# Performance work log

Hardware: AMD Instinct MI355X
Metric: run time of the kernel (lower is better)

Reference implementation:

```python
import jax, jax.numpy as jnp
import numpy as np

N = 50000
E = 500000
HID = 64
HEADS = 4
LAYERS = 4
CDIM = 8


def _p(key, shape, scale=0.05):
    return jax.random.normal(key, shape, dtype=jnp.float32) * scale


def setup_inputs() -> dict:
    key = jax.random.key(0)
    ks = jax.random.split(key, 32)
    x = jax.random.normal(ks[0], (N, 8), dtype=jnp.float32)
    src = jax.random.randint(ks[1], (E,), 0, N)
    dst = jax.random.randint(ks[2], (E,), 0, N)
    edge_index = jnp.stack([src, dst]).astype(jnp.int64)
    HC = HEADS * HID
    inp = {
        "x": x,
        "edge_index": edge_index,
        # encoder: Linear(8,64), ELU, Linear(64,64), ELU
        "enc_w1": _p(ks[3], (HID, 8)), "enc_b1": _p(ks[4], (HID,)),
        "enc_w2": _p(ks[5], (HID, HID)), "enc_b2": _p(ks[6], (HID,)),
        # per-layer TransformerConv params, stacked over layers
        "Wq": _p(ks[7], (LAYERS, HC, HID)), "bq": _p(ks[8], (LAYERS, HC)),
        "Wk": _p(ks[9], (LAYERS, HC, HID)), "bk": _p(ks[10], (LAYERS, HC)),
        "Wv": _p(ks[11], (LAYERS, HC, HID)), "bv": _p(ks[12], (LAYERS, HC)),
        "Ws": _p(ks[13], (LAYERS, HID, HID)), "bs": _p(ks[14], (LAYERS, HID)),
        # output MLP: 64->64->32->8
        "out_w1": _p(ks[15], (64, HID)), "out_b1": _p(ks[16], (64,)),
        "out_w2": _p(ks[17], (32, 64)), "out_b2": _p(ks[18], (32,)),
        "out_w3": _p(ks[19], (CDIM, 32)), "out_b3": _p(ks[20], (CDIM,)),
    }
    return inp


def transformer_conv(h, src, dst, Wq, bq, Wk, bk, Wv, bv, Ws, bs):
    """PyG TransformerConv, concat=False, root_weight=True, eval mode (no dropout)."""
    n = h.shape[0]
    q = (h @ Wq.T + bq).reshape(n, HEADS, HID)
    k = (h @ Wk.T + bk).reshape(n, HEADS, HID)
    v = (h @ Wv.T + bv).reshape(n, HEADS, HID)
    # per-edge multi-head scores: (E, H)
    alpha = jnp.einsum("ehd,ehd->eh", q[dst], k[src]) / np.sqrt(HID).astype(np.float32)
    # segment softmax over edges grouped by destination node
    amax = jax.ops.segment_max(alpha, dst, num_segments=n)          # (N, H)
    ex = jnp.exp(alpha - amax[dst])                                 # (E, H)
    denom = jax.ops.segment_sum(ex, dst, num_segments=n)           # (N, H)
    w = ex / denom[dst]                                             # (E, H)
    msg = v[src] * w[:, :, None]                                    # (E, H, C)
    agg = jax.ops.segment_sum(msg, dst, num_segments=n)            # (N, H, C)
    out = agg.mean(axis=1)                                          # concat=False -> head mean
    return out + h @ Ws.T + bs                                      # skip connection


def reference(x, edge_index, enc_w1, enc_b1, enc_w2, enc_b2,
              Wq, bq, Wk, bk, Wv, bv, Ws, bs,
              out_w1, out_b1, out_w2, out_b2, out_w3, out_b3):
    src, dst = edge_index[0], edge_index[1]
    elu = jax.nn.elu
    h = elu(x @ enc_w1.T + enc_b1)
    h = elu(h @ enc_w2.T + enc_b2)
    for l in range(LAYERS):
        h = elu(transformer_conv(h, src, dst, Wq[l], bq[l], Wk[l], bk[l],
                                 Wv[l], bv[l], Ws[l], bs[l]))
        # dropout is identity in eval mode
    o = elu(h @ out_w1.T + out_b1)
    o = elu(o @ out_w2.T + out_b2)
    o = o @ out_w3.T + out_b3
    return o
```

## Files before the change

### kernel.cpp

```cpp
#include <hip/hip_runtime.h>
#include <hip/hip_bf16.h>

#define N_NODES 50000
#define N_EDGES 500000
constexpr int HID = 64;
constexpr int HC  = 256;

typedef unsigned short u16;
typedef unsigned char u8;
typedef __attribute__((ext_vector_type(8))) __bf16 bf16x8;
typedef __attribute__((ext_vector_type(4))) float f32x4;
typedef __attribute__((ext_vector_type(2))) float f32x2;

__device__ __forceinline__ float b2f(u16 u) {
    union { unsigned int i; float f; } c; c.i = ((unsigned int)u) << 16; return c.f;
}
__device__ __forceinline__ u16 f2b(float f) {
    union { float f; unsigned int i; } c; c.f = f;
    unsigned int x = c.i;
    unsigned int lsb = (x >> 16) & 1u;
    x += 0x7fffu + lsb;
    return (u16)(x >> 16);
}
__device__ __forceinline__ float elu_f(float x) { return x > 0.f ? x : expm1f(x); }


__global__ __launch_bounds__(256) void init_kernel(int* __restrict__ cnt, int* __restrict__ cursor,
                                                   int* __restrict__ csr) {
    int i = blockIdx.x * 256 + threadIdx.x;
    if (i < N_NODES) { cnt[i] = 0; cursor[i] = 0; }
    if (blockIdx.x == 0 && threadIdx.x < 8) csr[N_EDGES + threadIdx.x] = 0;
}

__global__ __launch_bounds__(256) void detect_kernel(const int* __restrict__ ei, int* __restrict__ flag) {
    __shared__ int s[4];
    int t = threadIdx.x;
    int nz = ei[2 * t + 1] != 0;
    unsigned long long m = __ballot(nz);
    if ((t & 63) == 0) s[t >> 6] = (m != 0ull) ? 1 : 0;
    __syncthreads();
    if (t == 0) flag[0] = s[0] | s[1] | s[2] | s[3];
}

__global__ __launch_bounds__(256) void wcvt_kernel(const float* __restrict__ Wq, const float* __restrict__ Wk,
                                                   const float* __restrict__ Wv, const float* __restrict__ Wsk,
                                                   u16* __restrict__ w16) {
    int i = blockIdx.x * 256 + threadIdx.x;
    if (i >= 53248) return;
    const float* src; int off;
    if (i < 16384)      { src = Wq;  off = i; }
    else if (i < 32768) { src = Wk;  off = i - 16384; }
    else if (i < 49152) { src = Wv;  off = i - 32768; }
    else                { src = Wsk; off = i - 49152; }
    float4 v = ((const float4*)src)[off];
    ushort4 u; u.x = f2b(v.x); u.y = f2b(v.y); u.z = f2b(v.z); u.w = f2b(v.w);
    ((ushort4*)w16)[i] = u;
}

__global__ __launch_bounds__(256) void hist_kernel(const int* __restrict__ ei, const int* __restrict__ flag,
                                                   int* __restrict__ cnt) {
    int e = blockIdx.x * 256 + threadIdx.x;
    if (e < N_EDGES) {
        int d = flag[0] ? ei[N_EDGES + e] : ei[2 * N_EDGES + 2 * e];
        atomicAdd(&cnt[d], 1);
    }
}

__global__ __launch_bounds__(512) void scan1_kernel(const int* __restrict__ cnt,
                                                    int* __restrict__ row_start, int* __restrict__ bsum) {
    __shared__ int sc[512];
    int t = threadIdx.x;
    int i = blockIdx.x * 512 + t;
    int v = (i < N_NODES) ? cnt[i] : 0;
    sc[t] = v;
    __syncthreads();
    for (int off = 1; off < 512; off <<= 1) {
        int u = (t >= off) ? sc[t - off] : 0;
        __syncthreads();
        sc[t] += u;
        __syncthreads();
    }
    if (i < N_NODES) row_start[i] = sc[t] - v;
    if (t == 511) bsum[blockIdx.x] = sc[511];
}

__global__ __launch_bounds__(128) void scan2_kernel(int* __restrict__ bsum, int* __restrict__ row_start) {
    __shared__ int sc[128];
    const int NB = (N_NODES + 511) / 512;
    int t = threadIdx.x;
    int v = (t < NB) ? bsum[t] : 0;
    sc[t] = v;
    __syncthreads();
    for (int off = 1; off < 128; off <<= 1) {
        int u = (t >= off) ? sc[t - off] : 0;
        __syncthreads();
        sc[t] += u;
        __syncthreads();
    }
    if (t < NB) bsum[t] = sc[t] - v;
    if (t == 127) row_start[N_NODES] = sc[127];
}

__global__ __launch_bounds__(512) void scan3_kernel(int* __restrict__ row_start, const int* __restrict__ bsum) {
    int i = blockIdx.x * 512 + threadIdx.x;
    if (i < N_NODES) row_start[i] += bsum[blockIdx.x];
}

__global__ __launch_bounds__(256) void scatter_kernel(const int* __restrict__ ei, const int* __restrict__ flag,
                                const int* __restrict__ row_start, int* __restrict__ cursor,
                                int* __restrict__ csr_src) {
    int e = blockIdx.x * 256 + threadIdx.x;
    if (e < N_EDGES) {
        int isI32 = flag[0];
        int s = isI32 ? ei[e] : ei[2 * e];
        int d = isI32 ? ei[N_EDGES + e] : ei[2 * N_EDGES + 2 * e];
        int pos = row_start[d] + atomicAdd(&cursor[d], 1);
        csr_src[pos] = s;
    }
}

__global__ __launch_bounds__(256) void encoder_kernel(const float* __restrict__ x,
                               const float* __restrict__ w1, const float* __restrict__ b1,
                               const float* __restrict__ w2, const float* __restrict__ b2,
                               float* __restrict__ h) {
    __shared__ float xs[64 * 9];
    __shared__ float w1s[64 * 9];
    __shared__ u16 t1s[64 * 72];
    __shared__ u16 w2s[64 * 72];
    __shared__ float b1s[64], b2s[64];
    int t = threadIdx.x;
    int m0 = blockIdx.x * 64;

    if (t < 128) {
        int row = t >> 1, c = (t & 1) * 4;
        float4 val = make_float4(0.f, 0.f, 0.f, 0.f);
        if (m0 + row < N_NODES) val = *(const float4*)(x + (size_t)(m0 + row) * 8 + c);
        *(float4*)&xs[row * 9 + c] = val;
    }
    if (t >= 128 && t < 256) {
        int p = t - 128;
        int row = p >> 1, c = (p & 1) * 4;
        float4 val = *(const float4*)(w1 + row * 8 + c);
        *(float4*)&w1s[row * 9 + c] = val;
    }
    #pragma unroll
    for (int r = 0; r < 4; ++r) {
        int p = t + r * 256; int row = p >> 4, kc = (p & 15) * 4;
        float4 val = *(const float4*)(w2 + row * 64 + kc);
        ushort4 u; u.x = f2b(val.x); u.y = f2b(val.y); u.z = f2b(val.z); u.w = f2b(val.w);
        *(ushort4*)&w2s[row * 72 + kc] = u;
    }
    if (t < 64) { b1s[t] = b1[t]; b2s[t] = b2[t]; }
    __syncthreads();

    {
        int j = t & 63, sub = t >> 6;
        #pragma unroll
        for (int g = 0; g < 16; ++g) {
            int node = g * 4 + sub;
            float acc = b1s[j];
            #pragma unroll
            for (int m = 0; m < 8; ++m) acc += xs[node * 9 + m] * w1s[j * 9 + m];
            t1s[node * 72 + j] = f2b(elu_f(acc));
        }
    }
    __syncthreads();

    int wave = t >> 6, lane = t & 63;
    int lrow = lane & 15, quad = lane >> 4;
    int m_off = wave * 16;
    bf16x8 a0 = *(const bf16x8*)&t1s[(m_off + lrow) * 72 + quad * 8];
    bf16x8 a1 = *(const bf16x8*)&t1s[(m_off + lrow) * 72 + 32 + quad * 8];
    #pragma unroll
    for (int nsub = 0; nsub < 4; ++nsub) {
        bf16x8 b0 = *(const bf16x8*)&w2s[(nsub * 16 + lrow) * 72 + quad * 8];
        bf16x8 b1v = *(const bf16x8*)&w2s[(nsub * 16 + lrow) * 72 + 32 + quad * 8];
        f32x4 acc = {0.f, 0.f, 0.f, 0.f};
        acc = __builtin_amdgcn_mfma_f32_16x16x32_bf16(a0, b0, acc, 0, 0, 0);
        acc = __builtin_amdgcn_mfma_f32_16x16x32_bf16(a1, b1v, acc, 0, 0, 0);
        int col = nsub * 16 + lrow;
        float bias = b2s[col];
        #pragma unroll
        for (int r = 0; r < 4; ++r) {
            int row = m0 + m_off + quad * 4 + r;
            if (row < N_NODES) h[(size_t)row * 64 + col] = elu_f(acc[r] + bias);
        }
    }
}

__global__ __launch_bounds__(256) void proj_kernel(const float* __restrict__ h,
    const u16* __restrict__ wq16, const u16* __restrict__ wk16,
    const u16* __restrict__ wv16, const u16* __restrict__ wsk16,
    const float* __restrict__ bq, const float* __restrict__ bk,
    const float* __restrict__ bv, const float* __restrict__ bsk,
    int layer,
    u16* __restrict__ q, u8* __restrict__ kv, float* __restrict__ skip)
{
    __shared__ u16 as_tile[64 * 72];
    __shared__ u16 ws_tile[64 * 72];
    __shared__ float pool[64 * 68];
    u16* qst  = (u16*)pool;
    u8*  kvst = (u8*)pool;
    float* skst = pool;

    int t = threadIdx.x;
    int m0 = blockIdx.x * 64;

    #pragma unroll
    for (int r = 0; r < 4; ++r) {
        int p = t + r * 256; int row = p >> 4, kc = (p & 15) * 4;
        float4 val = make_float4(0.f, 0.f, 0.f, 0.f);
        if (m0 + row < N_NODES) val = *(const float4*)(h + (size_t)(m0 + row) * 64 + kc);
        ushort4 u; u.x = f2b(val.x); u.y = f2b(val.y); u.z = f2b(val.z); u.w = f2b(val.w);
        *(ushort4*)&as_tile[row * 72 + kc] = u;
    }
    __syncthreads();

    int wave = t >> 6, lane = t & 63;
    int lrow = lane & 15, quad = lane >> 4;
    bf16x8 a0 = *(const bf16x8*)&as_tile[(wave * 16 + lrow) * 72 + quad * 8];
    bf16x8 a1 = *(const bf16x8*)&as_tile[(wave * 16 + lrow) * 72 + 32 + quad * 8];

    const u16* Wq16  = wq16  + (size_t)layer * HC * HID;
    const u16* Wk16  = wk16  + (size_t)layer * HC * HID;
    const u16* Wv16  = wv16  + (size_t)layer * HC * HID;
    const u16* Wsk16 = wsk16 + (size_t)layer * HID * HID;
    const float* bqL  = bq  + layer * HC;
    const float* bkL  = bk  + layer * HC;
    const float* bvL  = bv  + layer * HC;
    const float* bskL = bsk + layer * HID;

    int nl = wave * 16 + lrow;

    auto tile_base = [&](int idx) -> const u16* {
        if (idx < 4) return Wq16 + (size_t)(idx * 64) * 64;
        if (idx < 12) {
            int p2 = idx - 4; int ctk = p2 >> 1;
            return ((p2 & 1) ? Wv16 : Wk16) + (size_t)(ctk * 64) * 64;
        }
        return Wsk16;
    };

    int p0 = t, p1 = t + 256;
    int g_off0 = (p0 >> 3) * 64 + (p0 & 7) * 8;
    int g_off1 = (p1 >> 3) * 64 + (p1 & 7) * 8;
    int l_off0 = (p0 >> 3) * 72 + (p0 & 7) * 8;
    int l_off1 = (p1 >> 3) * 72 + (p1 & 7) * 8;

    uint4 pre0 = *(const uint4*)(tile_base(0) + g_off0);
    uint4 pre1 = *(const uint4*)(tile_base(0) + g_off1);

    for (int idx = 0; idx < 13; ++idx) {
        const float* bt; int cbase; int mode;
        if (idx < 4)       { bt = bqL + idx * 64; cbase = idx * 64; mode = 0; }
        else if (idx < 12) { int p2 = idx - 4; int ctk = p2 >> 1; cbase = ctk * 64;
                             if ((p2 & 1) == 0) { bt = bkL + cbase; mode = 1; }
                             else               { bt = bvL + cbase; mode = 2; } }
        else               { bt = bskL; cbase = 0; mode = 3; }

        __syncthreads();
        *(uint4*)&ws_tile[l_off0] = pre0;
        *(uint4*)&ws_tile[l_off1] = pre1;
        if (idx + 1 < 13) {
            pre0 = *(const uint4*)(tile_base(idx + 1) + g_off0);
            pre1 = *(const uint4*)(tile_base(idx + 1) + g_off1);
        }
        __syncthreads();

        #pragma unroll
        for (int nsub = 0; nsub < 4; ++nsub) {
            bf16x8 w0 = *(const bf16x8*)&ws_tile[(nsub * 16 + lrow) * 72 + quad * 8];
            bf16x8 w1 = *(const bf16x8*)&ws_tile[(nsub * 16 + lrow) * 72 + 32 + quad * 8];
            f32x4 acc = {0.f, 0.f, 0.f, 0.f};
            acc = __builtin_amdgcn_mfma_f32_16x16x32_bf16(w0, a0, acc, 0, 0, 0);
            acc = __builtin_amdgcn_mfma_f32_16x16x32_bf16(w1, a1, acc, 0, 0, 0);
            float4 b4 = *(const float4*)(bt + nsub * 16 + quad * 4);
            if (mode == 0) {
                ushort4 o;
                o.x = f2b(acc[0] + b4.x); o.y = f2b(acc[1] + b4.y);
                o.z = f2b(acc[2] + b4.z); o.w = f2b(acc[3] + b4.w);
                *(ushort4*)&qst[nl * 72 + nsub * 16 + quad * 4] = o;
            } else if (mode == 1 || mode == 2) {
                float f0 = (acc[0] + b4.x) * 16.f, f1 = (acc[1] + b4.y) * 16.f;
                float f2v = (acc[2] + b4.z) * 16.f, f3v = (acc[3] + b4.w) * 16.f;
                int pk = __builtin_amdgcn_cvt_pk_fp8_f32(f0, f1, 0, false);
                pk = __builtin_amdgcn_cvt_pk_fp8_f32(f2v, f3v, pk, true);
                int g = nsub * 4 + quad;
                *(unsigned int*)&kvst[nl * 144 + g * 8 + (mode == 2 ? 4 : 0)] = (unsigned int)pk;
            } else {
                float4 o;
                o.x = acc[0] + b4.x; o.y = acc[1] + b4.y;
                o.z = acc[2] + b4.z; o.w = acc[3] + b4.w;
                *(float4*)&skst[nl * 68 + nsub * 16 + quad * 4] = o;
            }
        }

        if (mode == 0) {
            __syncthreads();
            #pragma unroll
            for (int it = 0; it < 2; ++it) {
                int p = t + it * 256; int row = p >> 3, ch = p & 7;
                int grow = m0 + row;
                if (grow < N_NODES)
                    *(uint4*)(q + (size_t)grow * 256 + cbase + ch * 8) = *(const uint4*)&qst[row * 72 + ch * 8];
            }
        } else if (mode == 2) {
            __syncthreads();
            #pragma unroll
            for (int it = 0; it < 2; ++it) {
                int p = t + it * 256; int row = p >> 3, ch = p & 7;
                int grow = m0 + row;
                if (grow < N_NODES)
                    *(uint4*)(kv + (size_t)grow * 512 + cbase * 2 + ch * 16) = *(const uint4*)&kvst[row * 144 + ch * 16];
            }
        } else if (mode == 3) {
            __syncthreads();
            int row = t >> 2, c0 = (t & 3) * 16;
            int grow = m0 + row;
            if (grow < N_NODES) {
                #pragma unroll
                for (int j = 0; j < 4; ++j)
                    *(float4*)(skip + (size_t)grow * 64 + c0 + j * 4) = *(const float4*)&skst[row * 68 + c0 + j * 4];
            }
        }
    }
}

__global__ __launch_bounds__(256) void attn_kernel(
    const u16* __restrict__ q, const u8* __restrict__ kv,
    const float* __restrict__ skip,
    const int* __restrict__ row_start, const int* __restrict__ csr_src,
    float* __restrict__ hout)
{
    int wave = threadIdx.x >> 6;
    int lane = threadIdx.x & 63;
    int n = blockIdx.x * 4 + wave;
    if (n >= N_NODES) return;
    const float SC = 0.0078125f * 1.44269504f;
    ushort4 q4 = ((const ushort4*)(q + (size_t)n * 256))[lane];
    float qf0 = b2f(q4.x) * SC, qf1 = b2f(q4.y) * SC, qf2 = b2f(q4.z) * SC, qf3 = b2f(q4.w) * SC;
    const u8* kvl = kv + lane * 8;
    float l = 0.f;
    float a0 = 0.f, a1 = 0.f, a2 = 0.f, a3 = 0.f;
    int e0 = row_start[n], e1 = row_start[n + 1];
    for (int e = e0; e < e1; e += 4) {
        int rem = e1 - e;
        int s0 = csr_src[e], s1 = csr_src[e + 1], s2 = csr_src[e + 2], s3 = csr_src[e + 3];
        uint2 c0 = *(const uint2*)(kvl + (size_t)s0 * 512);
        uint2 c1 = *(const uint2*)(kvl + (size_t)s1 * 512);
        uint2 c2 = *(const uint2*)(kvl + (size_t)s2 * 512);
        uint2 c3 = *(const uint2*)(kvl + (size_t)s3 * 512);
        f32x2 k0a = __builtin_amdgcn_cvt_pk_f32_fp8(c0.x, false), k0b = __builtin_amdgcn_cvt_pk_f32_fp8(c0.x, true);
        f32x2 k1a = __builtin_amdgcn_cvt_pk_f32_fp8(c1.x, false), k1b = __builtin_amdgcn_cvt_pk_f32_fp8(c1.x, true);
        f32x2 k2a = __builtin_amdgcn_cvt_pk_f32_fp8(c2.x, false), k2b = __builtin_amdgcn_cvt_pk_f32_fp8(c2.x, true);
        f32x2 k3a = __builtin_amdgcn_cvt_pk_f32_fp8(c3.x, false), k3b = __builtin_amdgcn_cvt_pk_f32_fp8(c3.x, true);
        float p0 = qf0 * k0a.x + qf1 * k0a.y + qf2 * k0b.x + qf3 * k0b.y;
        float p1 = qf0 * k1a.x + qf1 * k1a.y + qf2 * k1b.x + qf3 * k1b.y;
        float p2 = qf0 * k2a.x + qf1 * k2a.y + qf2 * k2b.x + qf3 * k2b.y;
        float p3 = qf0 * k3a.x + qf1 * k3a.y + qf2 * k3b.x + qf3 * k3b.y;
        p0 += __shfl_xor(p0, 1); p1 += __shfl_xor(p1, 1); p2 += __shfl_xor(p2, 1); p3 += __shfl_xor(p3, 1);
        p0 += __shfl_xor(p0, 2); p1 += __shfl_xor(p1, 2); p2 += __shfl_xor(p2, 2); p3 += __shfl_xor(p3, 2);
        p0 += __shfl_xor(p0, 4); p1 += __shfl_xor(p1, 4); p2 += __shfl_xor(p2, 4); p3 += __shfl_xor(p3, 4);
        p0 += __shfl_xor(p0, 8); p1 += __shfl_xor(p1, 8); p2 += __shfl_xor(p2, 8); p3 += __shfl_xor(p3, 8);
        float w0 = exp2f(p0);
        float w1 = rem > 1 ? exp2f(p1) : 0.f;
        float w2 = rem > 2 ? exp2f(p2) : 0.f;
        float w3 = rem > 3 ? exp2f(p3) : 0.f;
        l += (w0 + w1) + (w2 + w3);
        f32x2 v0a = __builtin_amdgcn_cvt_pk_f32_fp8(c0.y, false), v0b = __builtin_amdgcn_cvt_pk_f32_fp8(c0.y, true);
        f32x2 v1a = __builtin_amdgcn_cvt_pk_f32_fp8(c1.y, false), v1b = __builtin_amdgcn_cvt_pk_f32_fp8(c1.y, true);
        f32x2 v2a = __builtin_amdgcn_cvt_pk_f32_fp8(c2.y, false), v2b = __builtin_amdgcn_cvt_pk_f32_fp8(c2.y, true);
        f32x2 v3a = __builtin_amdgcn_cvt_pk_f32_fp8(c3.y, false), v3b = __builtin_amdgcn_cvt_pk_f32_fp8(c3.y, true);
        a0 += w0 * v0a.x + w1 * v1a.x + w2 * v2a.x + w3 * v3a.x;
        a1 += w0 * v0a.y + w1 * v1a.y + w2 * v2a.y + w3 * v3a.y;
        a2 += w0 * v0b.x + w1 * v1b.x + w2 * v2b.x + w3 * v3b.x;
        a3 += w0 * v0b.y + w1 * v1b.y + w2 * v2b.y + w3 * v3b.y;
    }
    float inv = l > 0.f ? 1.f / l : 0.f;
    a0 *= inv; a1 *= inv; a2 *= inv; a3 *= inv;
    a0 += __shfl_xor(a0, 16); a0 += __shfl_xor(a0, 32);
    a1 += __shfl_xor(a1, 16); a1 += __shfl_xor(a1, 32);
    a2 += __shfl_xor(a2, 16); a2 += __shfl_xor(a2, 32);
    a3 += __shfl_xor(a3, 16); a3 += __shfl_xor(a3, 32);
    if ((lane >> 4) == 0) {
        const float OS = 0.015625f;
        float4 sk = ((const float4*)(skip + (size_t)n * 64))[lane];
        float4 o;
        o.x = elu_f(OS * a0 + sk.x);
        o.y = elu_f(OS * a1 + sk.y);
        o.z = elu_f(OS * a2 + sk.z);
        o.w = elu_f(OS * a3 + sk.w);
        ((float4*)(hout + (size_t)n * 64))[lane] = o;
    }
}

__global__ __launch_bounds__(256) void mlp_kernel(const float* __restrict__ h,
    const float* __restrict__ w1, const float* __restrict__ b1,
    const float* __restrict__ w2, const float* __restrict__ b2,
    const float* __restrict__ w3, const float* __restrict__ b3,
    float* __restrict__ out)
{
    __shared__ u16 hs[64 * 72];
    __shared__ u16 w1s[64 * 72];
    __shared__ u16 t1s[64 * 72];
    __shared__ u16 w2s[32 * 72];
    __shared__ float t2s[64 * 33];
    __shared__ float w3s[8 * 33];
    __shared__ float b1s[64], b2s[32], b3s[8];
    int t = threadIdx.x;
    int m0 = blockIdx.x * 64;

    #pragma unroll
    for (int r = 0; r < 4; ++r) {
        int p = t + r * 256; int row = p >> 4, kc = (p & 15) * 4;
        float4 val = make_float4(0.f, 0.f, 0.f, 0.f);
        if (m0 + row < N_NODES) val = *(const float4*)(h + (size_t)(m0 + row) * 64 + kc);
        ushort4 u; u.x = f2b(val.x); u.y = f2b(val.y); u.z = f2b(val.z); u.w = f2b(val.w);
        *(ushort4*)&hs[row * 72 + kc] = u;
    }
    #pragma unroll
    for (int r = 0; r < 4; ++r) {
        int p = t + r * 256; int row = p >> 4, kc = (p & 15) * 4;
        float4 val = *(const float4*)(w1 + row * 64 + kc);
        ushort4 u; u.x = f2b(val.x); u.y = f2b(val.y); u.z = f2b(val.z); u.w = f2b(val.w);
        *(ushort4*)&w1s[row * 72 + kc] = u;
    }
    #pragma unroll
    for (int r = 0; r < 2; ++r) {
        int p = t + r * 256; int row = p >> 4, kc = (p & 15) * 4;
        float4 val = *(const float4*)(w2 + row * 64 + kc);
        ushort4 u; u.x = f2b(val.x); u.y = f2b(val.y); u.z = f2b(val.z); u.w = f2b(val.w);
        *(ushort4*)&w2s[row * 72 + kc] = u;
    }
    if (t < 8 * 32) { int r = t >> 5, c = t & 31; w3s[r * 33 + c] = w3[t]; }
    if (t < 64) b1s[t] = b1[t];
    if (t >= 64 && t < 96) b2s[t - 64] = b2[t - 64];
    if (t >= 96 && t < 104) b3s[t - 96] = b3[t - 96];
    __syncthreads();

    int wave = t >> 6, lane = t & 63;
    int lrow = lane & 15, quad = lane >> 4;
    int m_off = wave * 16;

    {
        bf16x8 a0 = *(const bf16x8*)&hs[(m_off + lrow) * 72 + quad * 8];
        bf16x8 a1 = *(const bf16x8*)&hs[(m_off + lrow) * 72 + 32 + quad * 8];
        #pragma unroll
        for (int nsub = 0; nsub < 4; ++nsub) {
            bf16x8 b0 = *(const bf16x8*)&w1s[(nsub * 16 + lrow) * 72 + quad * 8];
            bf16x8 b1v = *(const bf16x8*)&w1s[(nsub * 16 + lrow) * 72 + 32 + quad * 8];
            f32x4 acc = {0.f, 0.f, 0.f, 0.f};
            acc = __builtin_amdgcn_mfma_f32_16x16x32_bf16(a0, b0, acc, 0, 0, 0);
            acc = __builtin_amdgcn_mfma_f32_16x16x32_bf16(a1, b1v, acc, 0, 0, 0);
            int col = nsub * 16 + lrow;
            float bias = b1s[col];
            #pragma unroll
            for (int r = 0; r < 4; ++r) {
                int row = m_off + quad * 4 + r;
                t1s[row * 72 + col] = f2b(elu_f(acc[r] + bias));
            }
        }
    }
    __syncthreads();

    {
        bf16x8 a0 = *(const bf16x8*)&t1s[(m_off + lrow) * 72 + quad * 8];
        bf16x8 a1 = *(const bf16x8*)&t1s[(m_off + lrow) * 72 + 32 + quad * 8];
        #pragma unroll
        for (int nsub = 0; nsub < 2; ++nsub) {
            bf16x8 b0 = *(const bf16x8*)&w2s[(nsub * 16 + lrow) * 72 + quad * 8];
            bf16x8 b1v = *(const bf16x8*)&w2s[(nsub * 16 + lrow) * 72 + 32 + quad * 8];
            f32x4 acc = {0.f, 0.f, 0.f, 0.f};
            acc = __builtin_amdgcn_mfma_f32_16x16x32_bf16(a0, b0, acc, 0, 0, 0);
            acc = __builtin_amdgcn_mfma_f32_16x16x32_bf16(a1, b1v, acc, 0, 0, 0);
            int col = nsub * 16 + lrow;
            float bias = b2s[col];
            #pragma unroll
            for (int r = 0; r < 4; ++r) {
                int row = m_off + quad * 4 + r;
                t2s[row * 33 + col] = elu_f(acc[r] + bias);
            }
        }
    }
    __syncthreads();

    #pragma unroll
    for (int r = 0; r < 2; ++r) {
        int idx = t + r * 256;
        int node = idx >> 3, j = idx & 7;
        int row = m0 + node;
        if (row < N_NODES) {
            float acc = b3s[j];
            #pragma unroll
            for (int kk = 0; kk < 32; ++kk) acc += t2s[node * 33 + kk] * w3s[j * 33 + kk];
            out[(size_t)row * 8 + j] = acc;
        }
    }
}

extern "C" void kernel_launch(void* const* d_in, const int* in_sizes, int n_in,
                              void* d_out, int out_size, void* d_ws, size_t ws_size,
                              hipStream_t stream) {
    (void)in_sizes; (void)n_in; (void)out_size; (void)ws_size;
    const float* x   = (const float*)d_in[0];
    const int* ei    = (const int*)d_in[1];
    const float* ew1 = (const float*)d_in[2];
    const float* eb1 = (const float*)d_in[3];
    const float* ew2 = (const float*)d_in[4];
    const float* eb2 = (const float*)d_in[5];
    const float* Wq  = (const float*)d_in[6];
    const float* bq  = (const float*)d_in[7];
    const float* Wk  = (const float*)d_in[8];
    const float* bk  = (const float*)d_in[9];
    const float* Wv  = (const float*)d_in[10];
    const float* bv  = (const float*)d_in[11];
    const float* Wsk = (const float*)d_in[12];
    const float* bsk = (const float*)d_in[13];
    const float* ow1 = (const float*)d_in[14];
    const float* ob1 = (const float*)d_in[15];
    const float* ow2 = (const float*)d_in[16];
    const float* ob2 = (const float*)d_in[17];
    const float* ow3 = (const float*)d_in[18];
    const float* ob3 = (const float*)d_in[19];

    char* ws = (char*)d_ws;
    size_t off = 0;
    auto alloc = [&](size_t bytes) -> void* {
        void* p = ws + off;
        off += (bytes + 255) & ~(size_t)255;
        return p;
    };
    float* h0    = (float*)alloc((size_t)N_NODES * 64 * 4);
    float* h1    = (float*)alloc((size_t)N_NODES * 64 * 4);
    u16*   q     = (u16*)  alloc((size_t)N_NODES * 256 * 2);
    u8*    kv    = (u8*)   alloc((size_t)N_NODES * 512);
    float* skp   = (float*)alloc((size_t)N_NODES * 64 * 4);
    u16*   w16   = (u16*)  alloc((size_t)212992 * 2);
    int*   cnt   = (int*)  alloc((size_t)N_NODES * 4);
    int*   cursor= (int*)  alloc((size_t)N_NODES * 4);
    int*   rowst = (int*)  alloc((size_t)(N_NODES + 1) * 4);
    int*   csr   = (int*)  alloc((size_t)(N_EDGES + 8) * 4);
    int*   bsum  = (int*)  alloc(512);
    int*   flag  = (int*)  alloc(256);

    u16* wq16  = w16;
    u16* wk16  = w16 + 65536;
    u16* wv16  = w16 + 131072;
    u16* wsk16 = w16 + 196608;

    const int NB = (N_NODES + 511) / 512;

    init_kernel<<<(N_NODES + 255) / 256, 256, 0, stream>>>(cnt, cursor, csr);
    detect_kernel<<<1, 256, 0, stream>>>(ei, flag);
    wcvt_kernel<<<208, 256, 0, stream>>>(Wq, Wk, Wv, Wsk, w16);
    hist_kernel<<<(N_EDGES + 255) / 256, 256, 0, stream>>>(ei, flag, cnt);
    scan1_kernel<<<NB, 512, 0, stream>>>(cnt, rowst, bsum);
    scan2_kernel<<<1, 128, 0, stream>>>(bsum, rowst);
    scan3_kernel<<<NB, 512, 0, stream>>>(rowst, bsum);
    scatter_kernel<<<(N_EDGES + 255) / 256, 256, 0, stream>>>(ei, flag, rowst, cursor, csr);

    encoder_kernel<<<(N_NODES + 63) / 64, 256, 0, stream>>>(x, ew1, eb1, ew2, eb2, h0);

    float* hin = h0;
    float* hout = h1;
    for (int l = 0; l < 4; ++l) {
        proj_kernel<<<(N_NODES + 63) / 64, 256, 0, stream>>>(hin, wq16, wk16, wv16, wsk16,
                                                             bq, bk, bv, bsk, l, q, kv, skp);
        attn_kernel<<<(N_NODES + 3) / 4, 256, 0, stream>>>(q, kv, skp, rowst, csr, hout);
        float* tmp = hin; hin = hout; hout = tmp;
    }

    mlp_kernel<<<(N_NODES + 63) / 64, 256, 0, stream>>>(hin, ow1, ob1, ow2, ob2, ow3, ob3, (float*)d_out);
}
```

Measured before the change: 491.8 us.

## Process two degree-sorted nodes per wave in attention kernel

Adds a counting sort of nodes by in-degree (histogram, scan, scatter into a permutation) and changes the attention kernel so each 64-lane wave handles two nodes, one per 32-lane half. Each lane now loads 16 bytes of K/V and 8 query values per edge. Pairing nodes of similar degree is meant to limit divergence between the two halves while halving the number of waves and the per-edge shuffle depth. The cost is three extra small preprocessing kernels, an indirect node lookup, and scattered output writes in permuted order.

```diff
diff --git a/kernel.cpp b/kernel.cpp
--- a/kernel.cpp
+++ b/kernel.cpp
@@ -26,10 +26,12 @@
 
 
 __global__ __launch_bounds__(256) void init_kernel(int* __restrict__ cnt, int* __restrict__ cursor,
-                                                   int* __restrict__ csr) {
+                                                   int* __restrict__ csr,
+                                                   int* __restrict__ dbins, int* __restrict__ dcur) {
     int i = blockIdx.x * 256 + threadIdx.x;
     if (i < N_NODES) { cnt[i] = 0; cursor[i] = 0; }
     if (blockIdx.x == 0 && threadIdx.x < 8) csr[N_EDGES + threadIdx.x] = 0;
+    if (blockIdx.x == 0 && threadIdx.x < 64) { dbins[threadIdx.x] = 0; dcur[threadIdx.x] = 0; }
 }
 
 __global__ __launch_bounds__(256) void detect_kernel(const int* __restrict__ ei, int* __restrict__ flag) {
@@ -116,6 +118,41 @@
         int d = isI32 ? ei[N_EDGES + e] : ei[2 * N_EDGES + 2 * e];
         int pos = row_start[d] + atomicAdd(&cursor[d], 1);
         csr_src[pos] = s;
+    }
+}
+
+__global__ __launch_bounds__(256) void dhist_kernel(const int* __restrict__ cnt, int* __restrict__ dbins) {
+    __shared__ int lb[64];
+    int t = threadIdx.x;
+    if (t < 64) lb[t] = 0;
+    __syncthreads();
+    int i = blockIdx.x * 256 + t;
+    if (i < N_NODES) {
+        int d = cnt[i]; if (d > 63) d = 63;
+        atomicAdd(&lb[d], 1);
+    }
+    __syncthreads();
+    if (t < 64 && lb[t]) atomicAdd(&dbins[t], lb[t]);
+}
+
+__global__ __launch_bounds__(64) void dscan_kernel(const int* __restrict__ dbins, int* __restrict__ doffs) {
+    int t = threadIdx.x;
+    int v = dbins[t];
+    int s = v;
+    for (int off = 1; off < 64; off <<= 1) {
+        int u = __shfl_up(s, off);
+        if (t >= off) s += u;
+    }
+    doffs[t] = s - v;
+}
+
+__global__ __launch_bounds__(256) void dscatter_kernel(const int* __restrict__ cnt, const int* __restrict__ doffs,
+                                                       int* __restrict__ dcur, int* __restrict__ perm) {
+    int i = blockIdx.x * 256 + threadIdx.x;
+    if (i < N_NODES) {
+        int d = cnt[i]; if (d > 63) d = 63;
+        int pos = doffs[d] + atomicAdd(&dcur[d], 1);
+        perm[pos] = i;
     }
 }
 
@@ -330,67 +367,116 @@
     const u16* __restrict__ q, const u8* __restrict__ kv,
     const float* __restrict__ skip,
     const int* __restrict__ row_start, const int* __restrict__ csr_src,
+    const int* __restrict__ perm,
     float* __restrict__ hout)
 {
     int wave = threadIdx.x >> 6;
     int lane = threadIdx.x & 63;
-    int n = blockIdx.x * 4 + wave;
-    if (n >= N_NODES) return;
+    int half = lane >> 5;
+    int l32 = lane & 31;
+    int gw = blockIdx.x * 4 + wave;
+    int slot = 2 * gw + half;
+    bool valid = slot < N_NODES;
+    int n = valid ? perm[slot] : 0;
+
     const float SC = 0.0078125f * 1.44269504f;
-    ushort4 q4 = ((const ushort4*)(q + (size_t)n * 256))[lane];
-    float qf0 = b2f(q4.x) * SC, qf1 = b2f(q4.y) * SC, qf2 = b2f(q4.z) * SC, qf3 = b2f(q4.w) * SC;
-    const u8* kvl = kv + lane * 8;
+    float qf[8];
+    {
+        uint4 qr = *(const uint4*)(q + (size_t)n * 256 + l32 * 8);
+        const u16* qp = (const u16*)&qr;
+        #pragma unroll
+        for (int j = 0; j < 8; ++j) qf[j] = b2f(qp[j]) * SC;
+    }
+    int e0 = valid ? row_start[n] : 0;
+    int e1 = valid ? row_start[n + 1] : 0;
+    int ng = (e1 - e0 + 3) >> 2;
+    int ngo = __shfl_xor(ng, 32);
+    int ngmax = ng > ngo ? ng : ngo;
+    int elast = (e1 - 1 > e0) ? e1 - 1 : e0;
+
+    const u8* kvl = kv + l32 * 16;
     float l = 0.f;
-    float a0 = 0.f, a1 = 0.f, a2 = 0.f, a3 = 0.f;
-    int e0 = row_start[n], e1 = row_start[n + 1];
-    for (int e = e0; e < e1; e += 4) {
+    float a[8] = {};
+    for (int i = 0; i < ngmax; ++i) {
+        int e = e0 + 4 * i;
         int rem = e1 - e;
-        int s0 = csr_src[e], s1 = csr_src[e + 1], s2 = csr_src[e + 2], s3 = csr_src[e + 3];
-        uint2 c0 = *(const uint2*)(kvl + (size_t)s0 * 512);
-        uint2 c1 = *(const uint2*)(kvl + (size_t)s1 * 512);
-        uint2 c2 = *(const uint2*)(kvl + (size_t)s2 * 512);
-        uint2 c3 = *(const uint2*)(kvl + (size_t)s3 * 512);
-        f32x2 k0a = __builtin_amdgcn_cvt_pk_f32_fp8(c0.x, false), k0b = __builtin_amdgcn_cvt_pk_f32_fp8(c0.x, true);
-        f32x2 k1a = __builtin_amdgcn_cvt_pk_f32_fp8(c1.x, false), k1b = __builtin_amdgcn_cvt_pk_f32_fp8(c1.x, true);
-        f32x2 k2a = __builtin_amdgcn_cvt_pk_f32_fp8(c2.x, false), k2b = __builtin_amdgcn_cvt_pk_f32_fp8(c2.x, true);
-        f32x2 k3a = __builtin_amdgcn_cvt_pk_f32_fp8(c3.x, false), k3b = __builtin_amdgcn_cvt_pk_f32_fp8(c3.x, true);
-        float p0 = qf0 * k0a.x + qf1 * k0a.y + qf2 * k0b.x + qf3 * k0b.y;
-        float p1 = qf0 * k1a.x + qf1 * k1a.y + qf2 * k1b.x + qf3 * k1b.y;
-        float p2 = qf0 * k2a.x + qf1 * k2a.y + qf2 * k2b.x + qf3 * k2b.y;
-        float p3 = qf0 * k3a.x + qf1 * k3a.y + qf2 * k3b.x + qf3 * k3b.y;
+        int i0 = e     <= elast ? e     : elast;
+        int i1 = e + 1 <= elast ? e + 1 : elast;
+        int i2 = e + 2 <= elast ? e + 2 : elast;
+        int i3 = e + 3 <= elast ? e + 3 : elast;
+        int s0 = csr_src[i0], s1 = csr_src[i1], s2 = csr_src[i2], s3 = csr_src[i3];
+        uint4 c0 = *(const uint4*)(kvl + (size_t)s0 * 512);
+        uint4 c1 = *(const uint4*)(kvl + (size_t)s1 * 512);
+        uint4 c2 = *(const uint4*)(kvl + (size_t)s2 * 512);
+        uint4 c3 = *(const uint4*)(kvl + (size_t)s3 * 512);
+        float p0, p1, p2, p3;
+        {
+            f32x2 ka, kb, kc, kd;
+            ka = __builtin_amdgcn_cvt_pk_f32_fp8(c0.x, false); kb = __builtin_amdgcn_cvt_pk_f32_fp8(c0.x, true);
+            kc = __builtin_amdgcn_cvt_pk_f32_fp8(c0.z, false); kd = __builtin_amdgcn_cvt_pk_f32_fp8(c0.z, true);
+            p0 = qf[0]*ka.x + qf[1]*ka.y + qf[2]*kb.x + qf[3]*kb.y + qf[4]*kc.x + qf[5]*kc.y + qf[6]*kd.x + qf[7]*kd.y;
+            ka = __builtin_amdgcn_cvt_pk_f32_fp8(c1.x, false); kb = __builtin_amdgcn_cvt_pk_f32_fp8(c1.x, true);
+            kc = __builtin_amdgcn_cvt_pk_f32_fp8(c1.z, false); kd = __builtin_amdgcn_cvt_pk_f32_fp8(c1.z, true);
+            p1 = qf[0]*ka.x + qf[1]*ka.y + qf[2]*kb.x + qf[3]*kb.y + qf[4]*kc.x + qf[5]*kc.y + qf[6]*kd.x + qf[7]*kd.y;
+            ka = __builtin_amdgcn_cvt_pk_f32_fp8(c2.x, false); kb = __builtin_amdgcn_cvt_pk_f32_fp8(c2.x, true);
+            kc = __builtin_amdgcn_cvt_pk_f32_fp8(c2.z, false); kd = __builtin_amdgcn_cvt_pk_f32_fp8(c2.z, true);
+            p2 = qf[0]*ka.x + qf[1]*ka.y + qf[2]*kb.x + qf[3]*kb.y + qf[4]*kc.x + qf[5]*kc.y + qf[6]*kd.x + qf[7]*kd.y;
+            ka = __builtin_amdgcn_cvt_pk_f32_fp8(c3.x, false); kb = __builtin_amdgcn_cvt_pk_f32_fp8(c3.x, true);
+            kc = __builtin_amdgcn_cvt_pk_f32_fp8(c3.z, false); kd = __builtin_amdgcn_cvt_pk_f32_fp8(c3.z, true);
+            p3 = qf[0]*ka.x + qf[1]*ka.y + qf[2]*kb.x + qf[3]*kb.y + qf[4]*kc.x + qf[5]*kc.y + qf[6]*kd.x + qf[7]*kd.y;
+        }
         p0 += __shfl_xor(p0, 1); p1 += __shfl_xor(p1, 1); p2 += __shfl_xor(p2, 1); p3 += __shfl_xor(p3, 1);
         p0 += __shfl_xor(p0, 2); p1 += __shfl_xor(p1, 2); p2 += __shfl_xor(p2, 2); p3 += __shfl_xor(p3, 2);
         p0 += __shfl_xor(p0, 4); p1 += __shfl_xor(p1, 4); p2 += __shfl_xor(p2, 4); p3 += __shfl_xor(p3, 4);
-        p0 += __shfl_xor(p0, 8); p1 += __shfl_xor(p1, 8); p2 += __shfl_xor(p2, 8); p3 += __shfl_xor(p3, 8);
-        float w0 = exp2f(p0);
+        float w0 = rem > 0 ? exp2f(p0) : 0.f;
         float w1 = rem > 1 ? exp2f(p1) : 0.f;
         float w2 = rem > 2 ? exp2f(p2) : 0.f;
         float w3 = rem > 3 ? exp2f(p3) : 0.f;
         l += (w0 + w1) + (w2 + w3);
-        f32x2 v0a = __builtin_amdgcn_cvt_pk_f32_fp8(c0.y, false), v0b = __builtin_amdgcn_cvt_pk_f32_fp8(c0.y, true);
-        f32x2 v1a = __builtin_amdgcn_cvt_pk_f32_fp8(c1.y, false), v1b = __builtin_amdgcn_cvt_pk_f32_fp8(c1.y, true);
-        f32x2 v2a = __builtin_amdgcn_cvt_pk_f32_fp8(c2.y, false), v2b = __builtin_amdgcn_cvt_pk_f32_fp8(c2.y, true);
-        f32x2 v3a = __builtin_amdgcn_cvt_pk_f32_fp8(c3.y, false), v3b = __builtin_amdgcn_cvt_pk_f32_fp8(c3.y, true);
-        a0 += w0 * v0a.x + w1 * v1a.x + w2 * v2a.x + w3 * v3a.x;
-        a1 += w0 * v0a.y + w1 * v1a.y + w2 * v2a.y + w3 * v3a.y;
-        a2 += w0 * v0b.x + w1 * v1b.x + w2 * v2b.x + w3 * v3b.x;
-        a3 += w0 * v0b.y + w1 * v1b.y + w2 * v2b.y + w3 * v3b.y;
+        {
+            f32x2 va, vb;
+            va = __builtin_amdgcn_cvt_pk_f32_fp8(c0.y, false); vb = __builtin_amdgcn_cvt_pk_f32_fp8(c0.y, true);
+            a[0] += w0 * va.x; a[1] += w0 * va.y; a[2] += w0 * vb.x; a[3] += w0 * vb.y;
+            va = __builtin_amdgcn_cvt_pk_f32_fp8(c0.w, false); vb = __builtin_amdgcn_cvt_pk_f32_fp8(c0.w, true);
+            a[4] += w0 * va.x; a[5] += w0 * va.y; a[6] += w0 * vb.x; a[7] += w0 * vb.y;
+            va = __builtin_amdgcn_cvt_pk_f32_fp8(c1.y, false); vb = __builtin_amdgcn_cvt_pk_f32_fp8(c1.y, true);
+            a[0] += w1 * va.x; a[1] += w1 * va.y; a[2] += w1 * vb.x; a[3] += w1 * vb.y;
+            va = __builtin_amdgcn_cvt_pk_f32_fp8(c1.w, false); vb = __builtin_amdgcn_cvt_pk_f32_fp8(c1.w, true);
+            a[4] += w1 * va.x; a[5] += w1 * va.y; a[6] += w1 * vb.x; a[7] += w1 * vb.y;
+            va = __builtin_amdgcn_cvt_pk_f32_fp8(c2.y, false); vb = __builtin_amdgcn_cvt_pk_f32_fp8(c2.y, true);
+            a[0] += w2 * va.x; a[1] += w2 * va.y; a[2] += w2 * vb.x; a[3] += w2 * vb.y;
+            va = __builtin_amdgcn_cvt_pk_f32_fp8(c2.w, false); vb = __builtin_amdgcn_cvt_pk_f32_fp8(c2.w, true);
+            a[4] += w2 * va.x; a[5] += w2 * va.y; a[6] += w2 * vb.x; a[7] += w2 * vb.y;
+            va = __builtin_amdgcn_cvt_pk_f32_fp8(c3.y, false); vb = __builtin_amdgcn_cvt_pk_f32_fp8(c3.y, true);
+            a[0] += w3 * va.x; a[1] += w3 * va.y; a[2] += w3 * vb.x; a[3] += w3 * vb.y;
+            va = __builtin_amdgcn_cvt_pk_f32_fp8(c3.w, false); vb = __builtin_amdgcn_cvt_pk_f32_fp8(c3.w, true);
+            a[4] += w3 * va.x; a[5] += w3 * va.y; a[6] += w3 * vb.x; a[7] += w3 * vb.y;
+        }
     }
     float inv = l > 0.f ? 1.f / l : 0.f;
-    a0 *= inv; a1 *= inv; a2 *= inv; a3 *= inv;
-    a0 += __shfl_xor(a0, 16); a0 += __shfl_xor(a0, 32);
-    a1 += __shfl_xor(a1, 16); a1 += __shfl_xor(a1, 32);
-    a2 += __shfl_xor(a2, 16); a2 += __shfl_xor(a2, 32);
-    a3 += __shfl_xor(a3, 16); a3 += __shfl_xor(a3, 32);
-    if ((lane >> 4) == 0) {
+    #pragma unroll
+    for (int j = 0; j < 8; ++j) {
+        a[j] *= inv;
+        a[j] += __shfl_xor(a[j], 8);
+        a[j] += __shfl_xor(a[j], 16);
+    }
+    if ((l32 >> 3) == 0 && valid) {
         const float OS = 0.015625f;
-        float4 sk = ((const float4*)(skip + (size_t)n * 64))[lane];
-        float4 o;
-        o.x = elu_f(OS * a0 + sk.x);
-        o.y = elu_f(OS * a1 + sk.y);
-        o.z = elu_f(OS * a2 + sk.z);
-        o.w = elu_f(OS * a3 + sk.w);
-        ((float4*)(hout + (size_t)n * 64))[lane] = o;
+        const float* skp = skip + (size_t)n * 64 + l32 * 8;
+        float4 sk0 = *(const float4*)skp;
+        float4 sk1 = *(const float4*)(skp + 4);
+        float4 o0, o1;
+        o0.x = elu_f(OS * a[0] + sk0.x);
+        o0.y = elu_f(OS * a[1] + sk0.y);
+        o0.z = elu_f(OS * a[2] + sk0.z);
+        o0.w = elu_f(OS * a[3] + sk0.w);
+        o1.x = elu_f(OS * a[4] + sk1.x);
+        o1.y = elu_f(OS * a[5] + sk1.y);
+        o1.z = elu_f(OS * a[6] + sk1.z);
+        o1.w = elu_f(OS * a[7] + sk1.w);
+        float* hp = hout + (size_t)n * 64 + l32 * 8;
+        *(float4*)hp = o0;
+        *(float4*)(hp + 4) = o1;
     }
 }
 
@@ -540,6 +626,10 @@
     int*   cursor= (int*)  alloc((size_t)N_NODES * 4);
     int*   rowst = (int*)  alloc((size_t)(N_NODES + 1) * 4);
     int*   csr   = (int*)  alloc((size_t)(N_EDGES + 8) * 4);
+    int*   perm  = (int*)  alloc((size_t)N_NODES * 4);
+    int*   dbins = (int*)  alloc(64 * 4);
+    int*   doffs = (int*)  alloc(64 * 4);
+    int*   dcur  = (int*)  alloc(64 * 4);
     int*   bsum  = (int*)  alloc(512);
     int*   flag  = (int*)  alloc(256);
 
@@ -550,10 +640,13 @@
 
     const int NB = (N_NODES + 511) / 512;
 
-    init_kernel<<<(N_NODES + 255) / 256, 256, 0, stream>>>(cnt, cursor, csr);
+    init_kernel<<<(N_NODES + 255) / 256, 256, 0, stream>>>(cnt, cursor, csr, dbins, dcur);
     detect_kernel<<<1, 256, 0, stream>>>(ei, flag);
     wcvt_kernel<<<208, 256, 0, stream>>>(Wq, Wk, Wv, Wsk, w16);
     hist_kernel<<<(N_EDGES + 255) / 256, 256, 0, stream>>>(ei, flag, cnt);
+    dhist_kernel<<<(N_NODES + 255) / 256, 256, 0, stream>>>(cnt, dbins);
+    dscan_kernel<<<1, 64, 0, stream>>>(dbins, doffs);
+    dscatter_kernel<<<(N_NODES + 255) / 256, 256, 0, stream>>>(cnt, doffs, dcur, perm);
     scan1_kernel<<<NB, 512, 0, stream>>>(cnt, rowst, bsum);
     scan2_kernel<<<1, 128, 0, stream>>>(bsum, rowst);
     scan3_kernel<<<NB, 512, 0, stream>>>(rowst, bsum);
@@ -563,10 +656,11 @@
 
     float* hin = h0;
     float* hout = h1;
+    const int ATTN_BLOCKS = (N_NODES / 2 + 3) / 4;
     for (int l = 0; l < 4; ++l) {
         proj_kernel<<<(N_NODES + 63) / 64, 256, 0, stream>>>(hin, wq16, wk16, wv16, wsk16,
                                                              bq, bk, bv, bsk, l, q, kv, skp);
-        attn_kernel<<<(N_NODES + 3) / 4, 256, 0, stream>>>(q, kv, skp, rowst, csr, hout);
+        attn_kernel<<<ATTN_BLOCKS, 256, 0, stream>>>(q, kv, skp, rowst, csr, perm, hout);
         float* tmp = hin; hin = hout; hout = tmp;
     }
 
```

New measurement: 658.0 us. 1.34x slower.
